# Performance work log

Measured on AMD Instinct MI355X. Metric: run time of the kernel, lower is better.

The kernel has to match this reference:

```python
import jax, jax.numpy as jnp
import numpy as np

TEMPERATURE = 0.5
EPS = 1e-8  # matches torch CosineSimilarity eps


def setup_inputs() -> dict:
    key = jax.random.key(0)
    k1, k2 = jax.random.split(key)
    N, D = 4096, 256
    z1 = jax.random.normal(k1, (N, D), dtype=jnp.float32)
    z2 = jax.random.normal(k2, (N, D), dtype=jnp.float32)
    return {"z1": z1, "z2": z2}


def reference(z1, z2):
    N = z1.shape[0]
    z = jnp.concatenate([z1, z2], axis=0)            # [2N, D]
    norm = jnp.linalg.norm(z, axis=-1, keepdims=True)
    zn = z / jnp.maximum(norm, EPS)                  # L2-normalized
    sim = (zn @ zn.T) / TEMPERATURE                  # [2N, 2N] cosine sim / temp
    # mask self-similarity on the diagonal
    diag = jnp.eye(2 * N, dtype=bool)
    sim = jnp.where(diag, -jnp.inf, sim)
    # positive pair labels: row i pairs with i+N (first half) or i-N (second half)
    labels = jnp.concatenate([jnp.arange(N) + N, jnp.arange(N)])
    logp = jax.nn.log_softmax(sim, axis=-1)
    loss = -jnp.mean(logp[jnp.arange(2 * N), labels])
    return loss
```

## Files before the change

### kernel.cpp

```cpp
#include <hip/hip_runtime.h>
#include <hip/hip_bf16.h>


#define NROWS 8192
#define NHALF 4096
#define DDIM  256

typedef __bf16 bf16;
typedef __bf16 bf16x4 __attribute__((ext_vector_type(4)));
typedef __bf16 bf16x8 __attribute__((ext_vector_type(8)));
typedef float  f32x4  __attribute__((ext_vector_type(4)));

__constant__ const float kTwoLog2e = 2.8853900817779268f;
__constant__ const float kLn2      = 0.6931471805599453f;

__device__ __forceinline__ const float* zrow(const float* z1, const float* z2, int r) {
  return (r < NHALF) ? (z1 + (size_t)r * DDIM) : (z2 + (size_t)(r - NHALF) * DDIM);
}

__global__ void k_normalize(const float* __restrict__ z1, const float* __restrict__ z2,
                            bf16* __restrict__ zn, float* __restrict__ invn,
                            float* __restrict__ rowsum) {
  const int wave = threadIdx.x >> 6, lane = threadIdx.x & 63;
  const int row = blockIdx.x * 4 + wave;
  const float* src = zrow(z1, z2, row);
  f32x4 v = *(const f32x4*)(src + lane * 4);
  float ss = v.x * v.x + v.y * v.y + v.z * v.z + v.w * v.w;
#pragma unroll
  for (int off = 1; off < 64; off <<= 1) ss += __shfl_xor(ss, off);
  const float inv = 1.0f / fmaxf(sqrtf(ss), 1e-8f);
  bf16x4 o;
  o.x = (bf16)(v.x * inv); o.y = (bf16)(v.y * inv);
  o.z = (bf16)(v.z * inv); o.w = (bf16)(v.w * inv);
  *(bf16x4*)(zn + (size_t)row * DDIM + lane * 4) = o;
  if (lane == 0) { invn[row] = inv; rowsum[row] = 0.0f; }
}

#define BMG 128
#define BNG 32
#define TITERS 4
#define NTILES 2080

typedef const __attribute__((address_space(1))) unsigned int* as1_u32p;
typedef __attribute__((address_space(3))) unsigned int* as3_u32p;

__device__ __forceinline__ void load_lds16(const void* g, void* l) {
  __builtin_amdgcn_global_load_lds((as1_u32p)g, (as3_u32p)l, 16, 0, 0);
}

__global__ __launch_bounds__(256, 2) void k_gram(const bf16* __restrict__ zn,
                                                 float* __restrict__ rowsum) {
  __shared__ __align__(16) unsigned char ldsb[2][BNG * 512];
  const int tid  = threadIdx.x;
  const int wave = tid >> 6, lane = tid & 63;
  const int quad = lane >> 4, l15 = lane & 15;

  const int kb = blockIdx.x;
  int I = (int)((129.0f - sqrtf((float)(16641 - 8 * kb))) * 0.5f);
  while ((I + 1) * (129 - (I + 1)) / 2 <= kb) ++I;
  while (I * (129 - I) / 2 > kb) --I;
  const int J = I + (kb - I * (129 - I) / 2);
  const bool diag = (I == J);
  const int R0 = I * BMG + wave * 32;
  const int C0 = J * BMG;

  {
    const unsigned char* src0 = (const unsigned char*)(zn + (size_t)C0 * DDIM);
#pragma unroll
    for (int j = 0; j < 4; ++j) {
      const int p = (wave * 4 + j) * 64 + lane;
      const int r = p >> 5;
      const int q = (p & 31) ^ (r & 7);
      load_lds16(src0 + r * 512 + q * 16, &ldsb[0][(wave * 4 + j) * 1024]);
    }
  }

  bf16x8 a[2][8];
#pragma unroll
  for (int s = 0; s < 2; ++s) {
    const bf16x8* ap = (const bf16x8*)(zn + (size_t)(R0 + s * 16 + l15) * DDIM);
#pragma unroll
    for (int kk = 0; kk < 8; ++kk) a[s][kk] = ap[kk * 4 + quad];
  }

  float sum[2][4] = {{0.f, 0.f, 0.f, 0.f}, {0.f, 0.f, 0.f, 0.f}};
  float csum[TITERS][2];
  const f32x4 zero4 = {0.f, 0.f, 0.f, 0.f};

#pragma unroll
  for (int it = 0; it < TITERS; ++it) {
    __syncthreads();
    const unsigned char* bp = ldsb[it & 1];

    if (it + 1 < TITERS) {
      const unsigned char* srcn =
          (const unsigned char*)(zn + (size_t)(C0 + (it + 1) * BNG) * DDIM);
#pragma unroll
      for (int j = 0; j < 4; ++j) {
        const int p = (wave * 4 + j) * 64 + lane;
        const int r = p >> 5;
        const int q = (p & 31) ^ (r & 7);
        load_lds16(srcn + r * 512 + q * 16, &ldsb[(it + 1) & 1][(wave * 4 + j) * 1024]);
      }
    }

    f32x4 acc[2][2];
#pragma unroll
    for (int s = 0; s < 2; ++s) { acc[s][0] = zero4; acc[s][1] = zero4; }

#pragma unroll
    for (int kk = 0; kk < 8; ++kk) {
      bf16x8 b[2];
#pragma unroll
      for (int cs = 0; cs < 2; ++cs) {
        const int rb = cs * 16 + l15;
        const int q  = (kk * 4 + quad) ^ (rb & 7);
        b[cs] = *(const bf16x8*)(bp + rb * 512 + q * 16);
      }
#pragma unroll
      for (int s = 0; s < 2; ++s)
#pragma unroll
        for (int cs = 0; cs < 2; ++cs)
          acc[s][cs] =
              __builtin_amdgcn_mfma_f32_16x16x32_bf16(a[s][kk], b[cs], acc[s][cs], 0, 0, 0);
    }

    float c0 = 0.f, c1 = 0.f;
#pragma unroll
    for (int s = 0; s < 2; ++s)
#pragma unroll
      for (int r = 0; r < 4; ++r) {
        const float e0 = __builtin_amdgcn_exp2f(acc[s][0][r] * kTwoLog2e);
        const float e1 = __builtin_amdgcn_exp2f(acc[s][1][r] * kTwoLog2e);
        sum[s][r] += e0 + e1;
        c0 += e0; c1 += e1;
      }
    csum[it][0] = c0; csum[it][1] = c1;
  }

#pragma unroll
  for (int s = 0; s < 2; ++s)
#pragma unroll
    for (int r = 0; r < 4; ++r) {
      float v = sum[s][r];
      v += __shfl_xor(v, 1); v += __shfl_xor(v, 2);
      v += __shfl_xor(v, 4); v += __shfl_xor(v, 8);
      if (l15 == 0) atomicAdd(&rowsum[R0 + s * 16 + quad * 4 + r], v);
    }

  if (!diag) {
#pragma unroll
    for (int it = 0; it < TITERS; ++it)
#pragma unroll
      for (int cs = 0; cs < 2; ++cs) {
        float v = csum[it][cs];
        v += __shfl_xor(v, 16); v += __shfl_xor(v, 32);
        if (quad == 0) atomicAdd(&rowsum[C0 + it * BNG + cs * 16 + l15], v);
      }
  }
}

__global__ void k_finalize(const float* __restrict__ z1, const float* __restrict__ z2,
                           const bf16* __restrict__ zn, const float* __restrict__ invn,
                           const float* __restrict__ rowsum, float* __restrict__ contrib) {
  const int wave = threadIdx.x >> 6, lane = threadIdx.x & 63;
  const int row = blockIdx.x * 4 + wave;
  const int pr = (row < NHALF) ? row + NHALF : row - NHALF;

  f32x4 a4 = *(const f32x4*)(zrow(z1, z2, row) + lane * 4);
  f32x4 b4 = *(const f32x4*)(zrow(z1, z2, pr) + lane * 4);
  bf16x4 nb = *(const bf16x4*)(zn + (size_t)row * DDIM + lane * 4);

  float pd = a4.x * b4.x + a4.y * b4.y + a4.z * b4.z + a4.w * b4.w;
  float f0 = (float)nb.x, f1 = (float)nb.y, f2 = (float)nb.z, f3 = (float)nb.w;
  float nd = f0 * f0 + f1 * f1 + f2 * f2 + f3 * f3;
#pragma unroll
  for (int off = 1; off < 64; off <<= 1) {
    pd += __shfl_xor(pd, off);
    nd += __shfl_xor(nd, off);
  }
  if (lane == 0) {
    const float p = 2.0f * pd * invn[row] * invn[pr];
    const float dexp = __builtin_amdgcn_exp2f(kTwoLog2e * nd);
    const float lse = __builtin_amdgcn_logf(rowsum[row] - dexp) * kLn2;
    contrib[row] = lse - p;
  }
}

__global__ void k_reduce(const float* __restrict__ contrib, float* __restrict__ out) {
  const int wave = threadIdx.x >> 6, lane = threadIdx.x & 63;
  float acc = 0.0f;
  for (int i = threadIdx.x; i < NROWS; i += 256) acc += contrib[i];
#pragma unroll
  for (int off = 1; off < 64; off <<= 1) acc += __shfl_xor(acc, off);
  __shared__ float wsum[4];
  if (lane == 0) wsum[wave] = acc;
  __syncthreads();
  if (threadIdx.x == 0)
    out[0] = (wsum[0] + wsum[1] + wsum[2] + wsum[3]) * (1.0f / (float)NROWS);
}

extern "C" void kernel_launch(void* const* d_in, const int* in_sizes, int n_in,
                              void* d_out, int out_size, void* d_ws, size_t ws_size,
                              hipStream_t stream) {
  const float* z1 = (const float*)d_in[0];
  const float* z2 = (const float*)d_in[1];
  unsigned char* ws = (unsigned char*)d_ws;

  bf16* zn = (bf16*)ws;
  float* invn = (float*)(ws + (size_t)NROWS * DDIM * sizeof(bf16));
  float* rowsum = invn + NROWS;
  float* contrib = rowsum + NROWS;

  hipLaunchKernelGGL(k_normalize, dim3(NROWS / 4), dim3(256), 0, stream, z1, z2, zn, invn, rowsum);
  hipLaunchKernelGGL(k_gram, dim3(NTILES), dim3(256), 0, stream, zn, rowsum);
  hipLaunchKernelGGL(k_finalize, dim3(NROWS / 4), dim3(256), 0, stream, z1, z2, zn, invn, rowsum,
                     contrib);
  hipLaunchKernelGGL(k_reduce, dim3(1), dim3(256), 0, stream, contrib, (float*)d_out);
}
```

Baseline: 112.4 us.

## Prefetch whole column tile into LDS upfront with two 64-row halves

The gram kernel now loads the entire 128-row column tile into LDS as two 64-row halves, issuing both loads before compute starts. It replaces the four-step 32-row double-buffered loop with two steps, using explicit vmcnt waits and raw barriers. Each step runs 4 column subtiles per wave with raised wave priority during the MFMA loop, and the LDS swizzle widens to 16 slots. This cuts barrier count and load latency exposure, at the cost of 64KB of LDS per block, which may limit occupancy to the launch-bound target.

Result: slower. 118.9 us (+5.8%).

```diff
diff --git a/kernel.cpp b/kernel.cpp
--- a/kernel.cpp
+++ b/kernel.cpp
@@ -37,8 +37,6 @@
 }
 
 #define BMG 128
-#define BNG 32
-#define TITERS 4
 #define NTILES 2080
 
 typedef const __attribute__((address_space(1))) unsigned int* as1_u32p;
@@ -50,7 +48,7 @@
 
 __global__ __launch_bounds__(256, 2) void k_gram(const bf16* __restrict__ zn,
                                                  float* __restrict__ rowsum) {
-  __shared__ __align__(16) unsigned char ldsb[2][BNG * 512];
+  __shared__ __align__(16) unsigned char ldsb[2][64 * 512];
   const int tid  = threadIdx.x;
   const int wave = tid >> 6, lane = tid & 63;
   const int quad = lane >> 4, l15 = lane & 15;
@@ -65,13 +63,13 @@
   const int C0 = J * BMG;
 
   {
-    const unsigned char* src0 = (const unsigned char*)(zn + (size_t)C0 * DDIM);
-#pragma unroll
-    for (int j = 0; j < 4; ++j) {
-      const int p = (wave * 4 + j) * 64 + lane;
+    const unsigned char* s0 = (const unsigned char*)(zn + (size_t)C0 * DDIM);
+#pragma unroll
+    for (int j = 0; j < 8; ++j) {
+      const int p = (wave * 8 + j) * 64 + lane;
       const int r = p >> 5;
-      const int q = (p & 31) ^ (r & 7);
-      load_lds16(src0 + r * 512 + q * 16, &ldsb[0][(wave * 4 + j) * 1024]);
+      const int q = (p & 31) ^ (r & 15);
+      load_lds16(s0 + r * 512 + q * 16, &ldsb[0][(wave * 8 + j) * 1024]);
     }
   }
 
@@ -83,59 +81,72 @@
     for (int kk = 0; kk < 8; ++kk) a[s][kk] = ap[kk * 4 + quad];
   }
 
+  {
+    const unsigned char* s1 = (const unsigned char*)(zn + (size_t)(C0 + 64) * DDIM);
+#pragma unroll
+    for (int j = 0; j < 8; ++j) {
+      const int p = (wave * 8 + j) * 64 + lane;
+      const int r = p >> 5;
+      const int q = (p & 31) ^ (r & 15);
+      load_lds16(s1 + r * 512 + q * 16, &ldsb[1][(wave * 8 + j) * 1024]);
+    }
+  }
+  __builtin_amdgcn_sched_barrier(0);
+
   float sum[2][4] = {{0.f, 0.f, 0.f, 0.f}, {0.f, 0.f, 0.f, 0.f}};
-  float csum[TITERS][2];
+  float csum[2][4];
   const f32x4 zero4 = {0.f, 0.f, 0.f, 0.f};
 
 #pragma unroll
-  for (int it = 0; it < TITERS; ++it) {
-    __syncthreads();
-    const unsigned char* bp = ldsb[it & 1];
-
-    if (it + 1 < TITERS) {
-      const unsigned char* srcn =
-          (const unsigned char*)(zn + (size_t)(C0 + (it + 1) * BNG) * DDIM);
-#pragma unroll
-      for (int j = 0; j < 4; ++j) {
-        const int p = (wave * 4 + j) * 64 + lane;
-        const int r = p >> 5;
-        const int q = (p & 31) ^ (r & 7);
-        load_lds16(srcn + r * 512 + q * 16, &ldsb[(it + 1) & 1][(wave * 4 + j) * 1024]);
+  for (int h = 0; h < 2; ++h) {
+    if (h == 0) {
+      asm volatile("s_waitcnt vmcnt(8)" ::: "memory");
+    } else {
+      asm volatile("s_waitcnt vmcnt(0)" ::: "memory");
+    }
+    __builtin_amdgcn_s_barrier();
+    __builtin_amdgcn_sched_barrier(0);
+
+    const unsigned char* bp = ldsb[h];
+
+    f32x4 acc[2][4];
+#pragma unroll
+    for (int s = 0; s < 2; ++s)
+#pragma unroll
+      for (int cs = 0; cs < 4; ++cs) acc[s][cs] = zero4;
+
+    __builtin_amdgcn_s_setprio(1);
+#pragma unroll
+    for (int kk = 0; kk < 8; ++kk) {
+      bf16x8 b[4];
+#pragma unroll
+      for (int cs = 0; cs < 4; ++cs) {
+        const int rb = cs * 16 + l15;
+        const int sl = (kk * 4 + quad) ^ (rb & 15);
+        b[cs] = *(const bf16x8*)(bp + rb * 512 + sl * 16);
       }
-    }
-
-    f32x4 acc[2][2];
-#pragma unroll
-    for (int s = 0; s < 2; ++s) { acc[s][0] = zero4; acc[s][1] = zero4; }
-
-#pragma unroll
-    for (int kk = 0; kk < 8; ++kk) {
-      bf16x8 b[2];
-#pragma unroll
-      for (int cs = 0; cs < 2; ++cs) {
-        const int rb = cs * 16 + l15;
-        const int q  = (kk * 4 + quad) ^ (rb & 7);
-        b[cs] = *(const bf16x8*)(bp + rb * 512 + q * 16);
-      }
 #pragma unroll
       for (int s = 0; s < 2; ++s)
 #pragma unroll
-        for (int cs = 0; cs < 2; ++cs)
+        for (int cs = 0; cs < 4; ++cs)
           acc[s][cs] =
               __builtin_amdgcn_mfma_f32_16x16x32_bf16(a[s][kk], b[cs], acc[s][cs], 0, 0, 0);
     }
-
-    float c0 = 0.f, c1 = 0.f;
-#pragma unroll
-    for (int s = 0; s < 2; ++s)
-#pragma unroll
-      for (int r = 0; r < 4; ++r) {
-        const float e0 = __builtin_amdgcn_exp2f(acc[s][0][r] * kTwoLog2e);
-        const float e1 = __builtin_amdgcn_exp2f(acc[s][1][r] * kTwoLog2e);
-        sum[s][r] += e0 + e1;
-        c0 += e0; c1 += e1;
-      }
-    csum[it][0] = c0; csum[it][1] = c1;
+    __builtin_amdgcn_s_setprio(0);
+
+#pragma unroll
+    for (int cs = 0; cs < 4; ++cs) {
+      float c = 0.f;
+#pragma unroll
+      for (int s = 0; s < 2; ++s)
+#pragma unroll
+        for (int r = 0; r < 4; ++r) {
+          const float e = __builtin_amdgcn_exp2f(acc[s][cs][r] * kTwoLog2e);
+          sum[s][r] += e;
+          c += e;
+        }
+      csum[h][cs] = c;
+    }
   }
 
 #pragma unroll
@@ -150,12 +161,12 @@
 
   if (!diag) {
 #pragma unroll
-    for (int it = 0; it < TITERS; ++it)
-#pragma unroll
-      for (int cs = 0; cs < 2; ++cs) {
-        float v = csum[it][cs];
+    for (int h = 0; h < 2; ++h)
+#pragma unroll
+      for (int cs = 0; cs < 4; ++cs) {
+        float v = csum[h][cs];
         v += __shfl_xor(v, 16); v += __shfl_xor(v, 32);
-        if (quad == 0) atomicAdd(&rowsum[C0 + it * BNG + cs * 16 + l15], v);
+        if (quad == 0) atomicAdd(&rowsum[C0 + h * 64 + cs * 16 + l15], v);
       }
   }
 }
```
